# Kernel tuning notes

Hardware: AMD Instinct MI355X
Metric: run time of the kernel (lower is better)

Reference implementation:

```python
import jax, jax.numpy as jnp
import numpy as np


def setup_inputs() -> dict:
    key = jax.random.key(0)
    ks = jax.random.split(key, 8)
    n, c, h, w = 16, 256, 96, 96
    qk = 4
    x = jax.random.normal(ks[0], (n, c, h, w), dtype=jnp.float32)
    Wq = jax.random.normal(ks[1], (qk, c), dtype=jnp.float32) * 0.05
    Wk = jax.random.normal(ks[2], (qk, c), dtype=jnp.float32) * 0.05
    Wv = jax.random.normal(ks[3], (c, c), dtype=jnp.float32) * 0.05
    W1 = jax.random.normal(ks[4], (c, c), dtype=jnp.float32) * 0.05  # Linear(c, c//ratio), ratio=1
    W2 = jax.random.normal(ks[5], (c, c), dtype=jnp.float32) * 0.05  # Linear(c//ratio, c)
    gama = jax.random.normal(ks[6], (1,), dtype=jnp.float32) * 0.1
    return {"x": x, "Wq": Wq, "Wk": Wk, "Wv": Wv, "W1": W1, "W2": W2, "gama": gama}


def _se_gate(y, W1, W2):
    # SeNet_ChannelAttention: avg & max pool over HxW -> shared MLP -> sigmoid
    avg = jnp.mean(y, axis=(2, 3))            # [n, c]
    mx = jnp.max(y, axis=(2, 3))              # [n, c]
    def mlp(z):
        return jax.nn.relu(z @ W1.T) @ W2.T   # Linear weights are (out, in)
    return jax.nn.sigmoid(mlp(avg) + mlp(mx))  # [n, c]


def reference(x, Wq, Wk, Wv, W1, W2, gama):
    # 1x1 convs as pointwise channel projections
    Q = jnp.einsum('nchw,qc->nqhw', x, Wq)
    K = jnp.einsum('nchw,qc->nqhw', x, Wk)
    V = jnp.einsum('nchw,oc->nohw', x, Wv)

    # Row (width-axis) attention: per (n,h), queries/keys along w
    row_att = jax.nn.softmax(jnp.einsum('nqhw,nqhv->nhwv', Q, K), axis=-1)  # softmax over key pos v
    out1 = jnp.einsum('nchv,nhwv->nchw', V, row_att)

    # Column (height-axis) attention: per (n,w), queries/keys along h
    col_att = jax.nn.softmax(jnp.einsum('nqhw,nqgw->nwhg', Q, K), axis=-1)  # softmax over key pos g
    out2 = jnp.einsum('ncgw,nwhg->nchw', V, col_att)

    out = out1 + out2
    gate = _se_gate(out, W1, W2)              # [n, c]
    out = gate[:, :, None, None] * out
    return gama * out + x
```

## Files before the change

kernel.cpp:

```cpp
#include <hip/hip_runtime.h>
#include <hip/hip_fp16.h>

#define N_  16
#define C_  256
#define H_  96
#define W_  96
#define HW_ 9216
#define QK_ 4

struct alignas(8) h4 { __half2 a, b; };

__device__ inline void h4_unpack(h4 v, float* f) {
    float2 lo = __half22float2(v.a), hi = __half22float2(v.b);
    f[0] = lo.x; f[1] = lo.y; f[2] = hi.x; f[3] = hi.y;
}
__device__ inline h4 h4_pack(float a, float b, float c, float d) {
    h4 r; r.a = __floats2half2_rn(a, b); r.b = __floats2half2_rn(c, d); return r;
}

typedef __attribute__((ext_vector_type(8))) _Float16 f16x8;
typedef __attribute__((ext_vector_type(4))) float    f32x4;


__global__ __launch_bounds__(192) void ccca_qkt(
    const float* __restrict__ x, const float* __restrict__ Wq, const float* __restrict__ Wk,
    __half* __restrict__ xP, float* __restrict__ Qs, float* __restrict__ Ks)
{
    __shared__ float sW[8][C_];
    int t = threadIdx.x;
    int n = blockIdx.x / 12, gt = blockIdx.x % 12;
    for (int i = t; i < 8 * C_; i += 192)
        sW[i / C_][i % C_] = (i < 4 * C_) ? Wq[i] : Wk[i - 4 * C_];
    __syncthreads();
    int w = t % 96, gsub = t / 96;
    float accQ[4][4], accK[4][4];
    #pragma unroll
    for (int k = 0; k < 4; ++k)
        #pragma unroll
        for (int q = 0; q < 4; ++q) { accQ[k][q] = 0.f; accK[k][q] = 0.f; }
    const float* xb = x + (size_t)n * C_ * HW_ + (size_t)(gt * 8 + gsub * 4) * W_ + w;
    __half* xpd = xP + (((size_t)n * 12 + gt) * W_ + w) * 2048 + gsub * 4;
    for (int c = 0; c < C_; ++c) {
        float xv[4];
        #pragma unroll
        for (int k = 0; k < 4; ++k) xv[k] = xb[(size_t)c * HW_ + k * W_];
        *(h4*)(xpd + (size_t)c * 8) = h4_pack(xv[0], xv[1], xv[2], xv[3]);
        #pragma unroll
        for (int q = 0; q < QK_; ++q) {
            float wq = sW[q][c], wk = sW[4 + q][c];
            #pragma unroll
            for (int k = 0; k < 4; ++k) {
                accQ[k][q] = fmaf(wq, xv[k], accQ[k][q]);
                accK[k][q] = fmaf(wk, xv[k], accK[k][q]);
            }
        }
    }
    #pragma unroll
    for (int k = 0; k < 4; ++k) {
        int g = gt * 8 + gsub * 4 + k;
        #pragma unroll
        for (int q = 0; q < QK_; ++q) {
            Qs[(((size_t)n * QK_ + q) * H_ + g) * W_ + w] = accQ[k][q];
            Ks[(((size_t)n * QK_ + q) * H_ + g) * W_ + w] = accK[k][q];
        }
    }
}

__global__ __launch_bounds__(256) void ccca_rowm(
    const float* __restrict__ x, const float* __restrict__ Qs, const float* __restrict__ Ks,
    __half* __restrict__ Tb)
{
    __shared__ __half Xs[C_][104];
    __shared__ __half A1[W_][104];
    __shared__ float sQ[QK_][W_], sK[QK_][W_];
    int t = threadIdx.x;
    int n = blockIdx.x / H_, h = blockIdx.x % H_;
    const float* xb = x + (size_t)n * C_ * HW_ + (size_t)h * W_;
    for (int i = t; i < C_ * 24; i += 256) {
        int c = i / 24, v4 = (i % 24) * 4;
        float4 v = *(const float4*)(xb + (size_t)c * HW_ + v4);
        *(h4*)&Xs[c][v4] = h4_pack(v.x, v.y, v.z, v.w);
    }
    for (int i = t; i < 2 * QK_ * W_; i += 256) {
        int sel = i / (QK_ * W_), r = i % (QK_ * W_);
        int q = r / W_, w = r % W_;
        float v = (sel ? Ks : Qs)[(((size_t)n * QK_ + q) * H_ + h) * W_ + w];
        if (sel) sK[q][w] = v; else sQ[q][w] = v;
    }
    __syncthreads();
    for (int i = t; i < W_ * W_; i += 256) {
        int w = i / W_, v = i % W_;
        float s = 0.f;
        #pragma unroll
        for (int q = 0; q < QK_; ++q) s = fmaf(sQ[q][w], sK[q][v], s);
        A1[w][v] = __float2half(s);
    }
    __syncthreads();
    if (t < W_) {
        float m = -1e30f;
        for (int v = 0; v < W_; ++v) m = fmaxf(m, __half2float(A1[t][v]));
        float sum = 0.f;
        for (int v = 0; v < W_; ++v) {
            float e = __expf(__half2float(A1[t][v]) - m);
            sum += e; A1[t][v] = __float2half(e);
        }
        float inv = 1.f / sum;
        for (int v = 0; v < W_; ++v)
            A1[t][v] = __float2half(__half2float(A1[t][v]) * inv);
    }
    __syncthreads();
    int wd = t >> 6, lane = t & 63, ln15 = lane & 15, kg = lane >> 4;
    f32x4 acc[4][6];
    #pragma unroll
    for (int i = 0; i < 4; ++i)
        #pragma unroll
        for (int p = 0; p < 6; ++p) acc[i][p] = (f32x4){0.f, 0.f, 0.f, 0.f};
    #pragma unroll
    for (int kk = 0; kk < 3; ++kk) {
        f16x8 a[4], b[6];
        #pragma unroll
        for (int i = 0; i < 4; ++i)
            a[i] = *(const f16x8*)&Xs[64 * wd + 16 * i + ln15][kk * 32 + kg * 8];
        #pragma unroll
        for (int p = 0; p < 6; ++p)
            b[p] = *(const f16x8*)&A1[16 * p + ln15][kk * 32 + kg * 8];
        #pragma unroll
        for (int i = 0; i < 4; ++i)
            #pragma unroll
            for (int p = 0; p < 6; ++p)
                acc[i][p] = __builtin_amdgcn_mfma_f32_16x16x32_f16(a[i], b[p], acc[i][p], 0, 0, 0);
    }
    __half* Tn = Tb + ((size_t)n * H_ + h) * W_ * C_;
    #pragma unroll
    for (int i = 0; i < 4; ++i) {
        int c0 = 64 * wd + 16 * i + 4 * kg;
        #pragma unroll
        for (int p = 0; p < 6; ++p) {
            int w = 16 * p + ln15;
            *(h4*)(Tn + (size_t)w * C_ + c0) =
                h4_pack(acc[i][p][0], acc[i][p][1], acc[i][p][2], acc[i][p][3]);
        }
    }
}

__global__ __launch_bounds__(256) void ccca_colm(
    const __half* __restrict__ xP, const float* __restrict__ Qs, const float* __restrict__ Ks,
    __half* __restrict__ Tb)
{
    __shared__ __half Xs[C_][104];
    __shared__ __half A2[H_][104];
    __shared__ float sQ[QK_][H_], sK[QK_][H_];
    int t = threadIdx.x;
    int n = blockIdx.x / W_, w = blockIdx.x % W_;
    for (int i = t; i < 12 * C_; i += 256) {
        int gb = i >> 8, c = i & 255;
        f16x8 v = *(const f16x8*)(xP + (((size_t)n * 12 + gb) * W_ + w) * 2048 + (size_t)c * 8);
        *(f16x8*)&Xs[c][gb * 8] = v;
    }
    for (int i = t; i < 2 * QK_ * H_; i += 256) {
        int sel = i / (QK_ * H_), r = i % (QK_ * H_);
        int q = r / H_, g = r % H_;
        float v = (sel ? Ks : Qs)[(((size_t)n * QK_ + q) * H_ + g) * W_ + w];
        if (sel) sK[q][g] = v; else sQ[q][g] = v;
    }
    __syncthreads();
    for (int i = t; i < H_ * H_; i += 256) {
        int hh = i / H_, g = i % H_;
        float s = 0.f;
        #pragma unroll
        for (int q = 0; q < QK_; ++q) s = fmaf(sQ[q][hh], sK[q][g], s);
        A2[hh][g] = __float2half(s);
    }
    __syncthreads();
    if (t < H_) {
        float m = -1e30f;
        for (int g = 0; g < H_; ++g) m = fmaxf(m, __half2float(A2[t][g]));
        float sum = 0.f;
        for (int g = 0; g < H_; ++g) {
            float e = __expf(__half2float(A2[t][g]) - m);
            sum += e; A2[t][g] = __float2half(e);
        }
        float inv = 1.f / sum;
        for (int g = 0; g < H_; ++g)
            A2[t][g] = __float2half(__half2float(A2[t][g]) * inv);
    }
    __syncthreads();
    int wd = t >> 6, lane = t & 63, ln15 = lane & 15, kg = lane >> 4;
    f32x4 acc[6][4];
    #pragma unroll
    for (int i = 0; i < 6; ++i)
        #pragma unroll
        for (int p = 0; p < 4; ++p) acc[i][p] = (f32x4){0.f, 0.f, 0.f, 0.f};
    #pragma unroll
    for (int kk = 0; kk < 3; ++kk) {
        f16x8 a[6], b[4];
        #pragma unroll
        for (int i = 0; i < 6; ++i)
            a[i] = *(const f16x8*)&A2[16 * i + ln15][kk * 32 + kg * 8];
        #pragma unroll
        for (int p = 0; p < 4; ++p)
            b[p] = *(const f16x8*)&Xs[64 * wd + 16 * p + ln15][kk * 32 + kg * 8];
        #pragma unroll
        for (int i = 0; i < 6; ++i)
            #pragma unroll
            for (int p = 0; p < 4; ++p)
                acc[i][p] = __builtin_amdgcn_mfma_f32_16x16x32_f16(a[i], b[p], acc[i][p], 0, 0, 0);
    }
    __half* Tn = Tb + (size_t)n * HW_ * C_;
    #pragma unroll
    for (int i = 0; i < 6; ++i)
        #pragma unroll
        for (int p = 0; p < 4; ++p) {
            int c = 64 * wd + 16 * p + ln15;
            #pragma unroll
            for (int r = 0; r < 4; ++r) {
                int hh = 16 * i + 4 * kg + r;
                __half* ptr = Tn + ((size_t)hh * W_ + w) * C_ + c;
                *ptr = __float2half(__half2float(*ptr) + acc[i][p][r]);
            }
        }
}

__global__ __launch_bounds__(256) void ccca_cvtwv(
    const float* __restrict__ Wv, __half* __restrict__ Wvh)
{
    int gid = blockIdx.x * 256 + threadIdx.x;
    float4 v = ((const float4*)Wv)[gid];
    ((h4*)Wvh)[gid] = h4_pack(v.x, v.y, v.z, v.w);
}

__global__ __launch_bounds__(256) void ccca_wvm(
    const __half* __restrict__ Tb, const __half* __restrict__ Wvh,
    __half* __restrict__ OPb, float* __restrict__ psum, float* __restrict__ pmax)
{
    int t = threadIdx.x;
    int wd = t >> 6, lane = t & 63;
    int ln15 = lane & 15, kg = lane >> 4;
    int n = blockIdx.x / 144, tile = blockIdx.x % 144;

    const _Float16* Ab = (const _Float16*)Wvh + (size_t)(64 * wd + ln15) * C_ + kg * 8;
    const _Float16* Bb = (const _Float16*)Tb +
                         ((size_t)n * HW_ + tile * 64 + ln15) * C_ + kg * 8;

    f32x4 acc[4][4];
    #pragma unroll
    for (int i = 0; i < 4; ++i)
        #pragma unroll
        for (int p = 0; p < 4; ++p) acc[i][p] = (f32x4){0.f, 0.f, 0.f, 0.f};

    #pragma unroll
    for (int kk = 0; kk < 8; ++kk) {
        f16x8 a[4], b[4];
        #pragma unroll
        for (int i = 0; i < 4; ++i)
            a[i] = *(const f16x8*)(Ab + (size_t)i * 16 * C_ + kk * 32);
        #pragma unroll
        for (int p = 0; p < 4; ++p)
            b[p] = *(const f16x8*)(Bb + (size_t)p * 16 * C_ + kk * 32);
        #pragma unroll
        for (int i = 0; i < 4; ++i)
            #pragma unroll
            for (int p = 0; p < 4; ++p)
                acc[i][p] = __builtin_amdgcn_mfma_f32_16x16x32_f16(a[i], b[p], acc[i][p], 0, 0, 0);
    }

    __half* dst = OPb + (size_t)n * C_ * HW_;
    #pragma unroll
    for (int i = 0; i < 4; ++i) {
        #pragma unroll
        for (int r = 0; r < 4; ++r) {
            int c = 64 * wd + 16 * i + 4 * kg + r;
            #pragma unroll
            for (int p = 0; p < 4; ++p) {
                int px = tile * 64 + 16 * p + ln15;
                dst[(size_t)c * HW_ + px] = __float2half(acc[i][p][r]);
            }
        }
    }

    #pragma unroll
    for (int i = 0; i < 4; ++i) {
        float ps[4] = {0.f, 0.f, 0.f, 0.f};
        float pm[4] = {-1e30f, -1e30f, -1e30f, -1e30f};
        #pragma unroll
        for (int p = 0; p < 4; ++p)
            #pragma unroll
            for (int r = 0; r < 4; ++r) {
                ps[r] += acc[i][p][r];
                pm[r] = fmaxf(pm[r], acc[i][p][r]);
            }
        #pragma unroll
        for (int m = 1; m <= 8; m <<= 1)
            #pragma unroll
            for (int r = 0; r < 4; ++r) {
                ps[r] += __shfl_xor(ps[r], m);
                pm[r] = fmaxf(pm[r], __shfl_xor(pm[r], m));
            }
        if (ln15 == 0) {
            size_t base = ((size_t)n * 144 + tile) * C_ + 64 * wd + 16 * i + 4 * kg;
            #pragma unroll
            for (int r = 0; r < 4; ++r) { psum[base + r] = ps[r]; pmax[base + r] = pm[r]; }
        }
    }
}

__global__ __launch_bounds__(256) void ccca_gate2(
    const float* __restrict__ psum, const float* __restrict__ pmax,
    const float* __restrict__ W1, const float* __restrict__ W2,
    float* __restrict__ gate)
{
    __shared__ float sa[C_], sm[C_], hs[C_];
    int n = blockIdx.x, t = threadIdx.x;
    float s = 0.f, m = -1e30f;
    for (int i = 0; i < 144; ++i) {
        s += psum[((size_t)n * 144 + i) * C_ + t];
        m = fmaxf(m, pmax[((size_t)n * 144 + i) * C_ + t]);
    }
    sa[t] = s * (1.f / 9216.f);
    sm[t] = m;
    __syncthreads();
    const float* w1r = W1 + (size_t)t * C_;
    float aa = 0.f, am = 0.f;
    for (int i = 0; i < C_; ++i) { float wv = w1r[i]; aa = fmaf(wv, sa[i], aa); am = fmaf(wv, sm[i], am); }
    hs[t] = fmaxf(aa, 0.f) + fmaxf(am, 0.f);
    __syncthreads();
    const float* w2r = W2 + (size_t)t * C_;
    float g = 0.f;
    for (int i = 0; i < C_; ++i) g = fmaf(w2r[i], hs[i], g);
    gate[n * C_ + t] = 1.f / (1.f + __expf(-g));
}

__global__ __launch_bounds__(256) void ccca_final2(
    const float* __restrict__ x, const __half* __restrict__ OPb,
    const float* __restrict__ gate, const float* __restrict__ gama,
    float* __restrict__ out)
{
    float g0 = gama[0];
    const size_t total = (size_t)N_ * C_ * HW_ / 4;
    for (size_t i = (size_t)blockIdx.x * 256 + threadIdx.x; i < total; i += (size_t)gridDim.x * 256) {
        float4 xv = ((const float4*)x)[i];
        float ov[4];
        h4_unpack(((const h4*)OPb)[i], ov);
        size_t nc = (i * 4) / HW_;
        float sc = g0 * gate[nc];
        float4 r;
        r.x = fmaf(sc, ov[0], xv.x);
        r.y = fmaf(sc, ov[1], xv.y);
        r.z = fmaf(sc, ov[2], xv.z);
        r.w = fmaf(sc, ov[3], xv.w);
        ((float4*)out)[i] = r;
    }
}


__global__ __launch_bounds__(256) void ccca_qk(
    const float* __restrict__ x, const float* __restrict__ Wq,
    const float* __restrict__ Wk, float* __restrict__ Qo, float* __restrict__ Ko)
{
    __shared__ float sWq[QK_ * C_];
    __shared__ float sWk[QK_ * C_];
    int t = threadIdx.x;
    for (int i = t; i < QK_ * C_; i += 256) { sWq[i] = Wq[i]; sWk[i] = Wk[i]; }
    __syncthreads();
    int n = blockIdx.x / 36;
    int p = (blockIdx.x % 36) * 256 + t;
    const float* xp = x + (size_t)n * C_ * HW_ + p;
    float qa[QK_] = {0.f, 0.f, 0.f, 0.f};
    float ka[QK_] = {0.f, 0.f, 0.f, 0.f};
    for (int c = 0; c < C_; ++c) {
        float v = xp[(size_t)c * HW_];
        #pragma unroll
        for (int q = 0; q < QK_; ++q) {
            qa[q] = fmaf(v, sWq[q * C_ + c], qa[q]);
            ka[q] = fmaf(v, sWk[q * C_ + c], ka[q]);
        }
    }
    size_t base = (size_t)n * QK_ * HW_ + p;
    #pragma unroll
    for (int q = 0; q < QK_; ++q) { Qo[base + q * HW_] = qa[q]; Ko[base + q * HW_] = ka[q]; }
}

__global__ __launch_bounds__(256) void ccca_row(
    const float* __restrict__ x, const float* __restrict__ Qw,
    const float* __restrict__ Kw, float* __restrict__ out)
{
    __shared__ float sQ[QK_][W_];
    __shared__ float sK[QK_][W_];
    __shared__ float A[W_][W_ + 1];
    __shared__ float Xs[64][W_ + 1];
    int t = threadIdx.x;
    int n = blockIdx.x / H_;
    int h = blockIdx.x % H_;
    for (int i = t; i < QK_ * W_; i += 256) {
        int q = i / W_, w = i % W_;
        size_t off = ((size_t)n * QK_ + q) * HW_ + h * W_ + w;
        sQ[q][w] = Qw[off];
        sK[q][w] = Kw[off];
    }
    __syncthreads();
    for (int i = t; i < W_ * W_; i += 256) {
        int w = i / W_, v = i % W_;
        float s = 0.f;
        #pragma unroll
        for (int q = 0; q < QK_; ++q) s = fmaf(sQ[q][w], sK[q][v], s);
        A[w][v] = s;
    }
    __syncthreads();
    if (t < W_) {
        float m = -1e30f;
        for (int v = 0; v < W_; ++v) m = fmaxf(m, A[t][v]);
        float sum = 0.f;
        for (int v = 0; v < W_; ++v) { float e = __expf(A[t][v] - m); A[t][v] = e; sum += e; }
        float inv = 1.f / sum;
        for (int v = 0; v < W_; ++v) A[t][v] *= inv;
    }
    __syncthreads();
    int to = t >> 4, tw = t & 15;
    for (int ot = 0; ot < 4; ++ot) {
        for (int i = t; i < 64 * W_ / 4; i += 256) {
            int f = i * 4;
            int o = f / W_, v = f % W_;
            float4 val = *(const float4*)(x + (((size_t)n * C_ + ot * 64 + o) * H_ + h) * W_ + v);
            Xs[o][v] = val.x; Xs[o][v + 1] = val.y; Xs[o][v + 2] = val.z; Xs[o][v + 3] = val.w;
        }
        __syncthreads();
        float acc[4][6];
        #pragma unroll
        for (int i = 0; i < 4; ++i)
            #pragma unroll
            for (int j = 0; j < 6; ++j) acc[i][j] = 0.f;
        for (int v = 0; v < W_; ++v) {
            float xr[4], ar[6];
            #pragma unroll
            for (int i = 0; i < 4; ++i) xr[i] = Xs[to * 4 + i][v];
            #pragma unroll
            for (int j = 0; j < 6; ++j) ar[j] = A[tw * 6 + j][v];
            #pragma unroll
            for (int i = 0; i < 4; ++i)
                #pragma unroll
                for (int j = 0; j < 6; ++j) acc[i][j] = fmaf(xr[i], ar[j], acc[i][j]);
        }
        #pragma unroll
        for (int i = 0; i < 4; ++i) {
            size_t ob = (((size_t)n * C_ + ot * 64 + to * 4 + i) * H_ + h) * W_ + tw * 6;
            #pragma unroll
            for (int j = 0; j < 6; ++j) out[ob + j] = acc[i][j];
        }
        __syncthreads();
    }
}

__global__ __launch_bounds__(256) void ccca_col(
    const float* __restrict__ x, const float* __restrict__ Qw,
    const float* __restrict__ Kw, float* __restrict__ out)
{
    __shared__ float sQ[QK_][H_];
    __shared__ float sK[QK_][H_];
    __shared__ float A[H_][H_ + 1];
    __shared__ float Xc[64][H_ + 1];
    int t = threadIdx.x;
    int n = blockIdx.x / W_;
    int w = blockIdx.x % W_;
    for (int i = t; i < QK_ * H_; i += 256) {
        int q = i / H_, hh = i % H_;
        size_t off = ((size_t)n * QK_ + q) * HW_ + hh * W_ + w;
        sQ[q][hh] = Qw[off];
        sK[q][hh] = Kw[off];
    }
    __syncthreads();
    for (int i = t; i < H_ * H_; i += 256) {
        int hh = i / H_, g = i % H_;
        float s = 0.f;
        #pragma unroll
        for (int q = 0; q < QK_; ++q) s = fmaf(sQ[q][hh], sK[q][g], s);
        A[hh][g] = s;
    }
    __syncthreads();
    if (t < H_) {
        float m = -1e30f;
        for (int g = 0; g < H_; ++g) m = fmaxf(m, A[t][g]);
        float sum = 0.f;
        for (int g = 0; g < H_; ++g) { float e = __expf(A[t][g] - m); A[t][g] = e; sum += e; }
        float inv = 1.f / sum;
        for (int g = 0; g < H_; ++g) A[t][g] *= inv;
    }
    __syncthreads();
    int to = t >> 4, th = t & 15;
    for (int ot = 0; ot < 4; ++ot) {
        for (int i = t; i < 64 * H_; i += 256) {
            int o = i / H_, g = i % H_;
            Xc[o][g] = x[(((size_t)n * C_ + ot * 64 + o) * H_ + g) * W_ + w];
        }
        __syncthreads();
        float acc[4][6];
        #pragma unroll
        for (int i = 0; i < 4; ++i)
            #pragma unroll
            for (int j = 0; j < 6; ++j) acc[i][j] = 0.f;
        for (int g = 0; g < H_; ++g) {
            float xr[4], ar[6];
            #pragma unroll
            for (int i = 0; i < 4; ++i) xr[i] = Xc[to * 4 + i][g];
            #pragma unroll
            for (int j = 0; j < 6; ++j) ar[j] = A[th * 6 + j][g];
            #pragma unroll
            for (int i = 0; i < 4; ++i)
                #pragma unroll
                for (int j = 0; j < 6; ++j) acc[i][j] = fmaf(xr[i], ar[j], acc[i][j]);
        }
        #pragma unroll
        for (int i = 0; i < 4; ++i)
            #pragma unroll
            for (int j = 0; j < 6; ++j) {
                size_t ob = (((size_t)n * C_ + ot * 64 + to * 4 + i) * H_ + th * 6 + j) * W_ + w;
                out[ob] += acc[i][j];
            }
        __syncthreads();
    }
}

__global__ __launch_bounds__(256) void ccca_wv(
    const float* __restrict__ Wv, float* __restrict__ out)
{
    __shared__ float Ts[C_][64];
    int t = threadIdx.x;
    int n = blockIdx.x / 144;
    int p0 = (blockIdx.x % 144) * 64;
    float* base = out + (size_t)n * C_ * HW_ + p0;
    for (int i = t; i < C_ * 16; i += 256) {
        int o = i >> 4, p4 = (i & 15) << 2;
        *(float4*)&Ts[o][p4] = *(const float4*)(base + (size_t)o * HW_ + p4);
    }
    __syncthreads();
    int cb = t >> 4, pb = t & 15;
    float acc[16][4];
    #pragma unroll
    for (int j = 0; j < 16; ++j)
        #pragma unroll
        for (int p = 0; p < 4; ++p) acc[j][p] = 0.f;
    for (int o = 0; o < C_; o += 4) {
        float tvv[4][4];
        #pragma unroll
        for (int k = 0; k < 4; ++k) {
            float4 q = *(float4*)&Ts[o + k][pb * 4];
            tvv[k][0] = q.x; tvv[k][1] = q.y; tvv[k][2] = q.z; tvv[k][3] = q.w;
        }
        #pragma unroll
        for (int j = 0; j < 16; ++j) {
            float4 wv = *(const float4*)(Wv + (size_t)(cb * 16 + j) * C_ + o);
            float wvv[4] = {wv.x, wv.y, wv.z, wv.w};
            #pragma unroll
            for (int k = 0; k < 4; ++k)
                #pragma unroll
                for (int p = 0; p < 4; ++p)
                    acc[j][p] = fmaf(wvv[k], tvv[k][p], acc[j][p]);
        }
    }
    #pragma unroll
    for (int j = 0; j < 16; ++j) {
        float4 r; r.x = acc[j][0]; r.y = acc[j][1]; r.z = acc[j][2]; r.w = acc[j][3];
        *(float4*)(base + (size_t)(cb * 16 + j) * HW_ + pb * 4) = r;
    }
}

__global__ __launch_bounds__(256) void ccca_pool(
    const float* __restrict__ out, float* __restrict__ avg, float* __restrict__ mx)
{
    int nc = blockIdx.x;
    const float* p = out + (size_t)nc * HW_;
    int t = threadIdx.x;
    float s = 0.f, m = -1e30f;
    for (int i = t; i < HW_; i += 256) { float v = p[i]; s += v; m = fmaxf(m, v); }
    #pragma unroll
    for (int off = 32; off > 0; off >>= 1) {
        s += __shfl_down(s, off);
        m = fmaxf(m, __shfl_down(m, off));
    }
    __shared__ float ss[4], smx[4];
    int wv = t >> 6;
    if ((t & 63) == 0) { ss[wv] = s; smx[wv] = m; }
    __syncthreads();
    if (t == 0) {
        s = ss[0] + ss[1] + ss[2] + ss[3];
        m = fmaxf(fmaxf(smx[0], smx[1]), fmaxf(smx[2], smx[3]));
        avg[nc] = s * (1.f / 9216.f);
        mx[nc] = m;
    }
}

__global__ __launch_bounds__(256) void ccca_gate(
    const float* __restrict__ avg, const float* __restrict__ mx,
    const float* __restrict__ W1, const float* __restrict__ W2,
    float* __restrict__ gate)
{
    __shared__ float sa[C_], sm[C_], hs[C_];
    int n = blockIdx.x, t = threadIdx.x;
    sa[t] = avg[n * C_ + t];
    sm[t] = mx[n * C_ + t];
    __syncthreads();
    const float* w1r = W1 + (size_t)t * C_;
    float aa = 0.f, am = 0.f;
    for (int i = 0; i < C_; ++i) { float wv = w1r[i]; aa = fmaf(wv, sa[i], aa); am = fmaf(wv, sm[i], am); }
    hs[t] = fmaxf(aa, 0.f) + fmaxf(am, 0.f);
    __syncthreads();
    const float* w2r = W2 + (size_t)t * C_;
    float g = 0.f;
    for (int i = 0; i < C_; ++i) g = fmaf(w2r[i], hs[i], g);
    gate[n * C_ + t] = 1.f / (1.f + __expf(-g));
}

__global__ __launch_bounds__(256) void ccca_final(
    const float* __restrict__ x, const float* __restrict__ gate,
    const float* __restrict__ gama, float* __restrict__ out)
{
    float g0 = gama[0];
    const size_t total = (size_t)N_ * C_ * HW_ / 4;
    for (size_t i = (size_t)blockIdx.x * 256 + threadIdx.x; i < total; i += (size_t)gridDim.x * 256) {
        float4 o = ((const float4*)out)[i];
        float4 xv = ((const float4*)x)[i];
        size_t nc = (i * 4) / HW_;
        float sc = g0 * gate[nc];
        o.x = fmaf(sc, o.x, xv.x);
        o.y = fmaf(sc, o.y, xv.y);
        o.z = fmaf(sc, o.z, xv.z);
        o.w = fmaf(sc, o.w, xv.w);
        ((float4*)out)[i] = o;
    }
}


extern "C" void kernel_launch(void* const* d_in, const int* in_sizes, int n_in,
                              void* d_out, int out_size, void* d_ws, size_t ws_size,
                              hipStream_t stream)
{
    const float* x    = (const float*)d_in[0];
    const float* Wq   = (const float*)d_in[1];
    const float* Wk   = (const float*)d_in[2];
    const float* Wv   = (const float*)d_in[3];
    const float* W1   = (const float*)d_in[4];
    const float* W2   = (const float*)d_in[5];
    const float* gama = (const float*)d_in[6];
    float* out = (float*)d_out;
    char*  ws  = (char*)d_ws;

    const size_t WS_NEED3 = 155844608ull;

    if (ws_size >= WS_NEED3) {
        __half* xP   = (__half*)ws;
        __half* Tb   = (__half*)(ws + 75497472ull);
        float*  Qs   = (float*)(ws + 150994944ull);
        float*  Ks   = (float*)(ws + 153354240ull);
        __half* Wvh  = (__half*)(ws + 155713536ull);
        float*  psum = Qs;
        float*  pmax = Ks;
        float*  gate = (float*)Tb;
        __half* OPb  = xP;

        ccca_qkt  <<<N_ * 12, 192, 0, stream>>>(x, Wq, Wk, xP, Qs, Ks);
        ccca_cvtwv<<<64, 256, 0, stream>>>(Wv, Wvh);
        ccca_rowm <<<N_ * H_, 256, 0, stream>>>(x, Qs, Ks, Tb);
        ccca_colm <<<N_ * W_, 256, 0, stream>>>(xP, Qs, Ks, Tb);
        ccca_wvm  <<<N_ * 144, 256, 0, stream>>>(Tb, Wvh, OPb, psum, pmax);
        ccca_gate2<<<N_, 256, 0, stream>>>(psum, pmax, W1, W2, gate);
        ccca_final2<<<2048, 256, 0, stream>>>(x, OPb, gate, gama, out);
    } else {
        float* wsf = (float*)ws;
        const size_t QSZ = (size_t)N_ * QK_ * HW_;
        float* Qb   = wsf;
        float* Kb   = wsf + QSZ;
        float* avg  = wsf + 2 * QSZ;
        float* mx   = avg + N_ * C_;
        float* gate = mx + N_ * C_;
        ccca_qk  <<<N_ * 36, 256, 0, stream>>>(x, Wq, Wk, Qb, Kb);
        ccca_row <<<N_ * H_, 256, 0, stream>>>(x, Qb, Kb, out);
        ccca_col <<<N_ * W_, 256, 0, stream>>>(x, Qb, Kb, out);
        ccca_wv  <<<N_ * 144, 256, 0, stream>>>(Wv, out);
        ccca_pool<<<N_ * C_, 256, 0, stream>>>(out, avg, mx);
        ccca_gate<<<N_, 256, 0, stream>>>(avg, mx, W1, W2, gate);
        ccca_final<<<2048, 256, 0, stream>>>(x, gate, gama, out);
    }
}
```

Measured before the change: 701.8 us.

## Split Q/K projection over channel chunks with partial buffers and reduction kernel

The Q/K projection kernel now splits the 256-channel reduction into 8 chunks of 32, launching eight times as many blocks. Each block writes partial Q/K sums to scratch space reused from the Tb region, and a new kernel sums the partials. This raises parallelism in a launch that previously had too few blocks to fill the GPU. In exchange it adds extra global traffic for the partials and one more kernel launch.

```diff
diff --git a/kernel.cpp b/kernel.cpp
--- a/kernel.cpp
+++ b/kernel.cpp
@@ -7,6 +7,7 @@
 #define W_  96
 #define HW_ 9216
 #define QK_ 4
+#define QSZ_ 589824
 
 struct alignas(8) h4 { __half2 a, b; };
 
@@ -24,13 +25,19 @@
 
 __global__ __launch_bounds__(192) void ccca_qkt(
     const float* __restrict__ x, const float* __restrict__ Wq, const float* __restrict__ Wk,
-    __half* __restrict__ xP, float* __restrict__ Qs, float* __restrict__ Ks)
-{
-    __shared__ float sW[8][C_];
-    int t = threadIdx.x;
-    int n = blockIdx.x / 12, gt = blockIdx.x % 12;
-    for (int i = t; i < 8 * C_; i += 192)
-        sW[i / C_][i % C_] = (i < 4 * C_) ? Wq[i] : Wk[i - 4 * C_];
+    __half* __restrict__ xP, float* __restrict__ Qp, float* __restrict__ Kp)
+{
+    __shared__ float sW[8][32];
+    int t = threadIdx.x;
+    int blk = blockIdx.x;
+    int n = blk / 96;
+    int rem = blk % 96;
+    int gt = rem / 8, cc = rem % 8;
+    int c0 = cc * 32;
+    for (int i = t; i < 8 * 32; i += 192) {
+        int r = i / 32, c = i % 32;
+        sW[r][c] = (r < 4) ? Wq[r * C_ + c0 + c] : Wk[(r - 4) * C_ + c0 + c];
+    }
     __syncthreads();
     int w = t % 96, gsub = t / 96;
     float accQ[4][4], accK[4][4];
@@ -38,9 +45,11 @@
     for (int k = 0; k < 4; ++k)
         #pragma unroll
         for (int q = 0; q < 4; ++q) { accQ[k][q] = 0.f; accK[k][q] = 0.f; }
-    const float* xb = x + (size_t)n * C_ * HW_ + (size_t)(gt * 8 + gsub * 4) * W_ + w;
-    __half* xpd = xP + (((size_t)n * 12 + gt) * W_ + w) * 2048 + gsub * 4;
-    for (int c = 0; c < C_; ++c) {
+    const float* xb = x + (size_t)n * C_ * HW_ + (size_t)c0 * HW_
+                        + (size_t)(gt * 8 + gsub * 4) * W_ + w;
+    __half* xpd = xP + (((size_t)n * 12 + gt) * W_ + w) * 2048 + (size_t)c0 * 8 + gsub * 4;
+    #pragma unroll 2
+    for (int c = 0; c < 32; ++c) {
         float xv[4];
         #pragma unroll
         for (int k = 0; k < 4; ++k) xv[k] = xb[(size_t)c * HW_ + k * W_];
@@ -55,15 +64,32 @@
             }
         }
     }
+    size_t pbase = (size_t)cc * QSZ_;
     #pragma unroll
     for (int k = 0; k < 4; ++k) {
         int g = gt * 8 + gsub * 4 + k;
         #pragma unroll
         for (int q = 0; q < QK_; ++q) {
-            Qs[(((size_t)n * QK_ + q) * H_ + g) * W_ + w] = accQ[k][q];
-            Ks[(((size_t)n * QK_ + q) * H_ + g) * W_ + w] = accK[k][q];
-        }
-    }
+            size_t off = (((size_t)n * QK_ + q) * H_ + g) * W_ + w;
+            Qp[pbase + off] = accQ[k][q];
+            Kp[pbase + off] = accK[k][q];
+        }
+    }
+}
+
+__global__ __launch_bounds__(256) void ccca_qkred(
+    const float* __restrict__ Qp, const float* __restrict__ Kp,
+    float* __restrict__ Qs, float* __restrict__ Ks)
+{
+    size_t i = (size_t)blockIdx.x * 256 + threadIdx.x;
+    float q = 0.f, k = 0.f;
+    #pragma unroll
+    for (int cc = 0; cc < 8; ++cc) {
+        q += Qp[(size_t)cc * QSZ_ + i];
+        k += Kp[(size_t)cc * QSZ_ + i];
+    }
+    Qs[i] = q;
+    Ks[i] = k;
 }
 
 __global__ __launch_bounds__(256) void ccca_rowm(
@@ -651,12 +677,15 @@
         float*  Qs   = (float*)(ws + 150994944ull);
         float*  Ks   = (float*)(ws + 153354240ull);
         __half* Wvh  = (__half*)(ws + 155713536ull);
+        float*  Qp   = (float*)(ws + 75497472ull);
+        float*  Kp   = (float*)(ws + 75497472ull + 8ull * QSZ_ * 4ull);
         float*  psum = Qs;
         float*  pmax = Ks;
         float*  gate = (float*)Tb;
         __half* OPb  = xP;
 
-        ccca_qkt  <<<N_ * 12, 192, 0, stream>>>(x, Wq, Wk, xP, Qs, Ks);
+        ccca_qkt  <<<N_ * 96, 192, 0, stream>>>(x, Wq, Wk, xP, Qp, Kp);
+        ccca_qkred<<<QSZ_ / 256, 256, 0, stream>>>(Qp, Kp, Qs, Ks);
         ccca_cvtwv<<<64, 256, 0, stream>>>(Wv, Wvh);
         ccca_rowm <<<N_ * H_, 256, 0, stream>>>(x, Qs, Ks, Tb);
         ccca_colm <<<N_ * W_, 256, 0, stream>>>(xP, Qs, Ks, Tb);
```

New measurement: 698.7 us. No clear change (-0.4%).

## Fuse Q/K projection into row attention kernel and parallelize xP transpose

Applied to the files above, without the earlier changes.

Moves the Q/K 1x1 projection out of the transpose kernel and into the row-attention kernel, where x is already staged in shared memory as half, so Q/K reuse that load. The transpose kernel becomes a pure x->xP relayout, launched with 8x more blocks and using a swizzled LDS tile to avoid bank conflicts. The old launch had only 192 blocks doing a serial 256-channel loop. Q/K are now computed from fp16-rounded x, which slightly changes precision.

```diff
diff --git a/kernel.cpp b/kernel.cpp
--- a/kernel.cpp
+++ b/kernel.cpp
@@ -7,6 +7,7 @@
 #define W_  96
 #define HW_ 9216
 #define QK_ 4
+#define QSZ_ 589824
 
 struct alignas(8) h4 { __half2 a, b; };
 
@@ -22,57 +23,50 @@
 typedef __attribute__((ext_vector_type(4))) float    f32x4;
 
 
-__global__ __launch_bounds__(192) void ccca_qkt(
+__global__ __launch_bounds__(256) void ccca_qkt(
+    const float* __restrict__ x, __half* __restrict__ xP)
+{
+    __shared__ __half L[128 * 132];
+    int t = threadIdx.x;
+    int blk = blockIdx.x;
+    int n = blk / 96;
+    int rem = blk % 96;
+    int gt = rem / 8, cc = rem % 8;
+    __half* xpb = xP + ((size_t)n * 12 + gt) * W_ * 2048;
+    #pragma unroll
+    for (int pass = 0; pass < 2; ++pass) {
+        int cb = cc * 32 + pass * 16;
+        if (pass) __syncthreads();
+        for (int i = t; i < 128 * 24; i += 256) {
+            int row = i / 24, j = i % 24;
+            int c = row >> 3;
+            int g = row & 7;
+            int w0 = j * 4;
+            float4 v = *(const float4*)(x +
+                ((size_t)(n * C_ + cb + c) * H_ + (gt * 8 + g)) * (size_t)W_ + w0);
+            *(h4*)&L[row * 132 + (w0 ^ (c << 2))] = h4_pack(v.x, v.y, v.z, v.w);
+        }
+        __syncthreads();
+        for (int i = t; i < 96 * 32; i += 256) {
+            int w = i >> 5, piece = i & 31;
+            int c = piece >> 1, g0 = (piece & 1) << 2;
+            const __half* Lr = &L[(c * 8 + g0) * 132 + (w ^ (c << 2))];
+            h4 o;
+            o.a = __halves2half2(Lr[0],   Lr[132]);
+            o.b = __halves2half2(Lr[264], Lr[396]);
+            *(h4*)(xpb + (size_t)w * 2048 + (cb + c) * 8 + g0) = o;
+        }
+    }
+}
+
+__global__ __launch_bounds__(256) void ccca_rowm(
     const float* __restrict__ x, const float* __restrict__ Wq, const float* __restrict__ Wk,
-    __half* __restrict__ xP, float* __restrict__ Qs, float* __restrict__ Ks)
-{
-    __shared__ float sW[8][C_];
-    int t = threadIdx.x;
-    int n = blockIdx.x / 12, gt = blockIdx.x % 12;
-    for (int i = t; i < 8 * C_; i += 192)
-        sW[i / C_][i % C_] = (i < 4 * C_) ? Wq[i] : Wk[i - 4 * C_];
-    __syncthreads();
-    int w = t % 96, gsub = t / 96;
-    float accQ[4][4], accK[4][4];
-    #pragma unroll
-    for (int k = 0; k < 4; ++k)
-        #pragma unroll
-        for (int q = 0; q < 4; ++q) { accQ[k][q] = 0.f; accK[k][q] = 0.f; }
-    const float* xb = x + (size_t)n * C_ * HW_ + (size_t)(gt * 8 + gsub * 4) * W_ + w;
-    __half* xpd = xP + (((size_t)n * 12 + gt) * W_ + w) * 2048 + gsub * 4;
-    for (int c = 0; c < C_; ++c) {
-        float xv[4];
-        #pragma unroll
-        for (int k = 0; k < 4; ++k) xv[k] = xb[(size_t)c * HW_ + k * W_];
-        *(h4*)(xpd + (size_t)c * 8) = h4_pack(xv[0], xv[1], xv[2], xv[3]);
-        #pragma unroll
-        for (int q = 0; q < QK_; ++q) {
-            float wq = sW[q][c], wk = sW[4 + q][c];
-            #pragma unroll
-            for (int k = 0; k < 4; ++k) {
-                accQ[k][q] = fmaf(wq, xv[k], accQ[k][q]);
-                accK[k][q] = fmaf(wk, xv[k], accK[k][q]);
-            }
-        }
-    }
-    #pragma unroll
-    for (int k = 0; k < 4; ++k) {
-        int g = gt * 8 + gsub * 4 + k;
-        #pragma unroll
-        for (int q = 0; q < QK_; ++q) {
-            Qs[(((size_t)n * QK_ + q) * H_ + g) * W_ + w] = accQ[k][q];
-            Ks[(((size_t)n * QK_ + q) * H_ + g) * W_ + w] = accK[k][q];
-        }
-    }
-}
-
-__global__ __launch_bounds__(256) void ccca_rowm(
-    const float* __restrict__ x, const float* __restrict__ Qs, const float* __restrict__ Ks,
-    __half* __restrict__ Tb)
+    float* __restrict__ Qs, float* __restrict__ Ks, __half* __restrict__ Tb)
 {
     __shared__ __half Xs[C_][104];
     __shared__ __half A1[W_][104];
     __shared__ float sQ[QK_][W_], sK[QK_][W_];
+    float* sW = (float*)&A1[0][0];
     int t = threadIdx.x;
     int n = blockIdx.x / H_, h = blockIdx.x % H_;
     const float* xb = x + (size_t)n * C_ * HW_ + (size_t)h * W_;
@@ -81,11 +75,27 @@
         float4 v = *(const float4*)(xb + (size_t)c * HW_ + v4);
         *(h4*)&Xs[c][v4] = h4_pack(v.x, v.y, v.z, v.w);
     }
-    for (int i = t; i < 2 * QK_ * W_; i += 256) {
-        int sel = i / (QK_ * W_), r = i % (QK_ * W_);
-        int q = r / W_, w = r % W_;
-        float v = (sel ? Ks : Qs)[(((size_t)n * QK_ + q) * H_ + h) * W_ + w];
-        if (sel) sK[q][w] = v; else sQ[q][w] = v;
+    for (int i = t; i < 512; i += 256) {
+        float4 v = (i < 256) ? ((const float4*)Wq)[i] : ((const float4*)Wk)[i - 256];
+        ((float4*)sW)[i] = v;
+    }
+    __syncthreads();
+    if (t < 192) {
+        int w = t % 96, sel = t / 96;
+        float acc[4] = {0.f, 0.f, 0.f, 0.f};
+        const float* wr = sW + sel * 4 * C_;
+        for (int c = 0; c < C_; ++c) {
+            float xv = __half2float(Xs[c][w]);
+            #pragma unroll
+            for (int q = 0; q < 4; ++q)
+                acc[q] = fmaf(wr[q * C_ + c], xv, acc[q]);
+        }
+        #pragma unroll
+        for (int q = 0; q < 4; ++q) {
+            size_t off = (((size_t)n * QK_ + q) * H_ + h) * W_ + w;
+            if (sel) { sK[q][w] = acc[q]; Ks[off] = acc[q]; }
+            else     { sQ[q][w] = acc[q]; Qs[off] = acc[q]; }
+        }
     }
     __syncthreads();
     for (int i = t; i < W_ * W_; i += 256) {
@@ -656,9 +666,9 @@
         float*  gate = (float*)Tb;
         __half* OPb  = xP;
 
-        ccca_qkt  <<<N_ * 12, 192, 0, stream>>>(x, Wq, Wk, xP, Qs, Ks);
+        ccca_rowm <<<N_ * H_, 256, 0, stream>>>(x, Wq, Wk, Qs, Ks, Tb);
+        ccca_qkt  <<<N_ * 96, 256, 0, stream>>>(x, xP);
         ccca_cvtwv<<<64, 256, 0, stream>>>(Wv, Wvh);
-        ccca_rowm <<<N_ * H_, 256, 0, stream>>>(x, Qs, Ks, Tb);
         ccca_colm <<<N_ * W_, 256, 0, stream>>>(xP, Qs, Ks, Tb);
         ccca_wvm  <<<N_ * 144, 256, 0, stream>>>(Tb, Wvh, OPb, psum, pmax);
         ccca_gate2<<<N_, 256, 0, stream>>>(psum, pmax, W1, W2, gate);
```

Measured after the change: 639.3 us. 1.1x faster.
